# Performance work log

Measured on AMD Instinct MI355X. Metric: run time of the kernel, lower is better.

## Reference

```python
import jax, jax.numpy as jnp
import numpy as np

B, T_SRC, T_TGT, H = 256, 128, 32, 512


def setup_inputs() -> dict:
    key = jax.random.key(0)
    ks = jax.random.split(key, 16)
    bound = 1.0 / np.sqrt(H)  # PyTorch LSTM default init range

    def w(k, *sh):
        return jax.random.uniform(k, sh, jnp.float32, -bound, bound)

    return {
        "src": jax.random.normal(ks[0], (B, T_SRC, 1), jnp.float32),
        # encoder layer 0 (input_dim=1) and layer 1 (input_dim=H); gate order i,f,g,o
        "enc_w_ih0": w(ks[1], 4 * H, 1), "enc_w_hh0": w(ks[2], 4 * H, H), "enc_b0": w(ks[3], 4 * H),
        "enc_w_ih1": w(ks[4], 4 * H, H), "enc_w_hh1": w(ks[5], 4 * H, H), "enc_b1": w(ks[6], 4 * H),
        # decoder layers
        "dec_w_ih0": w(ks[7], 4 * H, 1), "dec_w_hh0": w(ks[8], 4 * H, H), "dec_b0": w(ks[9], 4 * H),
        "dec_w_ih1": w(ks[10], 4 * H, H), "dec_w_hh1": w(ks[11], 4 * H, H), "dec_b1": w(ks[12], 4 * H),
        # output projection Linear(H, 1)
        "proj_w": w(ks[13], 1, H), "proj_b": w(ks[14], 1),
        "tgt_len": T_TGT,
    }


def _cell(gx, h, c, w_hh):
    # gx: precomputed x @ w_ih.T + b; PyTorch gate order i, f, g, o
    gates = gx + h @ w_hh.T
    i, f, g, o = jnp.split(gates, 4, axis=-1)
    c = jax.nn.sigmoid(f) * c + jax.nn.sigmoid(i) * jnp.tanh(g)
    h = jax.nn.sigmoid(o) * jnp.tanh(c)
    return h, c


def _run_layer(xs, w_ih, w_hh, b):
    # xs: (B, T, in) -> (outputs (B,T,H), final h (B,H), final c (B,H))
    Bb, Hh = xs.shape[0], w_hh.shape[1]
    gx = jnp.einsum('bti,gi->btg', xs, w_ih) + b  # hoist input GEMM out of the scan

    def step(carry, g_t):
        h, c = carry
        h, c = _cell(g_t, h, c, w_hh)
        return (h, c), h

    z = jnp.zeros((Bb, Hh), xs.dtype)
    (h, c), hs = jax.lax.scan(step, (z, z), gx.transpose(1, 0, 2))
    return hs.transpose(1, 0, 2), h, c


def reference(src, enc_w_ih0, enc_w_hh0, enc_b0, enc_w_ih1, enc_w_hh1, enc_b1,
              dec_w_ih0, dec_w_hh0, dec_b0, dec_w_ih1, dec_w_hh1, dec_b1,
              proj_w, proj_b, tgt_len):
    # ---- encoder: 2-layer LSTM over src, keep final (h, c) per layer ----
    hs0, h0, c0 = _run_layer(src, enc_w_ih0, enc_w_hh0, enc_b0)
    _, h1, c1 = _run_layer(hs0, enc_w_ih1, enc_w_hh1, enc_b1)

    last = src[:, -1, :]  # (B, 1), last observed value

    def dec_step(carry, _):
        last, h0, c0, h1, c1 = carry
        gx0 = last @ dec_w_ih0.T + dec_b0
        h0, c0 = _cell(gx0, h0, c0, dec_w_hh0)
        gx1 = h0 @ dec_w_ih1.T + dec_b1
        h1, c1 = _cell(gx1, h1, c1, dec_w_hh1)
        y = h1 @ proj_w.T + proj_b  # (B, 1)
        # original feeds out.detach() as the next input
        return (jax.lax.stop_gradient(y), h0, c0, h1, c1), y

    _, ys = jax.lax.scan(dec_step, (last, h0, c0, h1, c1), None, length=tgt_len)
    return ys.transpose(1, 0, 2)  # (B, tgt_len, 1)
```

## Files before the change

### kernel.cpp

```cpp
#include <hip/hip_runtime.h>
#include <cstdint>
#include <cstddef>

#define BN 256
#define HN 512
#define TSN 128
#define TTN 32
#define NSL 16
#define SRN 128

typedef __fp16 f16;
typedef __fp16 f16x8 __attribute__((ext_vector_type(8)));
typedef float  f32x4 __attribute__((ext_vector_type(4)));
typedef float  f32x2 __attribute__((ext_vector_type(2)));
typedef unsigned int u32;
typedef unsigned int u32x2 __attribute__((ext_vector_type(2)));

static constexpr size_t WQ_OFF  = 0;
static constexpr size_t WQ_MAT  = (size_t)NSL*SRN*HN*2;
static constexpr size_t HS0_OFF = WQ_OFF + 6*WQ_MAT;
static constexpr size_t HS_SLOT = (size_t)BN*HN*2;
static constexpr size_t H1_OFF  = HS0_OFF + 129*HS_SLOT;
static constexpr size_t H0_OFF  = H1_OFF + 2*HS_SLOT;
static constexpr size_t YP_OFF  = H0_OFF + 2*HS_SLOT;
static constexpr size_t BAR_OFF = YP_OFF + (size_t)BN*NSL*4;

__device__ __forceinline__ float sigm(float x){ return 1.f/(1.f+__expf(-x)); }
__device__ __forceinline__ float tanh_(float x){
  float t = __expf(-2.f*fabsf(x));
  float r = (1.f-t)/(1.f+t);
  return x<0.f ? -r : r;
}

__device__ __forceinline__ f16x8 ldg16_cv(const f16* p){
  f32x4 r;
  asm volatile("global_load_dwordx4 %0, %1, off sc1" : "=v"(r) : "v"(p));
  return __builtin_bit_cast(f16x8, r);
}
__device__ __forceinline__ f32x2 ldg8f_cv(const float* p){
  f32x2 r;
  asm volatile("global_load_dwordx2 %0, %1, off sc1" : "=v"(r) : "v"(p));
  return r;
}
__device__ __forceinline__ void stg8_cv(f16* p, u32x2 v){
  asm volatile("global_store_dwordx2 %0, %1, off sc1" :: "v"(p), "v"(v) : "memory");
}
__device__ __forceinline__ void stg4f_cv(float* p, float v){
  asm volatile("global_store_dword %0, %1, off sc1" :: "v"(p), "v"(v) : "memory");
}
__device__ __forceinline__ void vmwait(){
  asm volatile("s_waitcnt vmcnt(0)" ::: "memory");
  __builtin_amdgcn_sched_barrier(0);
}
__device__ __forceinline__ void wait_k(const int* fb, int wv, int target){
  const int l = threadIdx.x & 63;
  const int* p = fb + (((wv<<2) | ((l>>2)&3))<<2) + (l&3);
  int v;
  do {
    asm volatile("global_load_dword %0, %1, off sc1\n\ts_waitcnt vmcnt(0)"
                 : "=v"(v) : "v"(p) : "memory");
  } while (!__all(v >= target));
  __builtin_amdgcn_sched_barrier(0);
}
__device__ __forceinline__ void wait_row(const int* fb, int wv, int target){
  const int l = threadIdx.x & 63;
  const int* p = fb + ((l&15)<<2) + wv;
  int v;
  do {
    asm volatile("global_load_dword %0, %1, off sc1\n\ts_waitcnt vmcnt(0)"
                 : "=v"(v) : "v"(p) : "memory");
  } while (!__all(v >= target));
  __builtin_amdgcn_sched_barrier(0);
}
__device__ __forceinline__ void post_wave(int* slot, int v){
  asm volatile("s_waitcnt vmcnt(0)" ::: "memory");
  __builtin_amdgcn_sched_barrier(0);
  if ((threadIdx.x & 63) == 0)
    asm volatile("global_store_dword %0, %1, off sc1" :: "v"(slot), "v"(v) : "memory");
}
__device__ __forceinline__ void post_wave2(int* sa, int va, int* sb, int vb){
  asm volatile("s_waitcnt vmcnt(0)" ::: "memory");
  __builtin_amdgcn_sched_barrier(0);
  if ((threadIdx.x & 63) == 0){
    asm volatile("global_store_dword %0, %1, off sc1" :: "v"(sa), "v"(va) : "memory");
    asm volatile("global_store_dword %0, %1, off sc1" :: "v"(sb), "v"(vb) : "memory");
  }
}

__device__ __forceinline__ void load_bslice(const f16* wsl, int lane, int wv, f16x8 (&bw)[8][4]){
  const int rr = lane & 15;
  const int ko = ((lane>>4)<<3) + wv*128;
  #pragma unroll
  for (int nt=0; nt<8; ++nt){
    const f16* p = wsl + (size_t)(nt*16+rr)*HN + ko;
    #pragma unroll
    for (int kk=0; kk<4; ++kk) bw[nt][kk] = *(const f16x8*)(p + kk*32);
  }
}
template<int MT>
__device__ __forceinline__ void load_a_cv(const f16* ab, int lane, int wv, f16x8 (&A)[MT][4]){
  const int rr = lane & 15;
  const int ko = ((lane>>4)<<3) + wv*128;
  #pragma unroll
  for (int mt=0; mt<MT; ++mt){
    const f16* p = ab + (size_t)(mt*16+rr)*HN + ko;
    #pragma unroll
    for (int kk=0; kk<4; ++kk) A[mt][kk] = ldg16_cv(p + kk*32);
  }
}
__device__ __forceinline__ void mfma_row(const f16x8 (&A)[4], const f16x8 (&bw)[8][4],
                                         f32x4 (&acc)[8]){
  #pragma unroll
  for (int kk=0; kk<4; ++kk)
    #pragma unroll
    for (int nt=0; nt<8; ++nt)
      acc[nt] = __builtin_amdgcn_mfma_f32_16x16x32_f16(A[kk], bw[nt][kk], acc[nt], 0, 0, 0);
}
__device__ __forceinline__ void wpart1(float (*gS)[32][132], const f32x4 (&acc)[8], int lane, int wv, int mt){
  const int c0 = lane & 15, r0 = (lane>>4)*4;
  #pragma unroll
  for (int nt=0; nt<8; ++nt)
    #pragma unroll
    for (int i=0; i<4; ++i)
      gS[wv][mt*16+r0+i][nt*16+c0] = acc[nt][i];
}
__device__ __forceinline__ float gsum(const float (*gS)[32][132], int row, int r){
  return gS[0][row][r] + gS[1][row][r] + gS[2][row][r] + gS[3][row][r];
}

__global__ void k_init(uint8_t* ws){
  const int i = blockIdx.x*256 + threadIdx.x;
  float* a = (float*)(ws + HS0_OFF);
  float* b = (float*)(ws + H1_OFF);
  int*   c = (int*)(ws + BAR_OFF);
  a[i] = 0.f;
  b[i] = 0.f;
  if (i < 2048) c[i] = 0;
}
__global__ void k_wconv(const float* s0, const float* s1, const float* s2,
                        const float* s3, const float* s4, const float* s5, f16* dst){
  const int i = blockIdx.x*256 + threadIdx.x;
  const int k = i & 511, r = (i>>9)&127, j = (i>>16)&15, m = i>>20;
  const float* s = (m==0)?s0:(m==1)?s1:(m==2)?s2:(m==3)?s3:(m==4)?s4:s5;
  const int R = (r>>5)*512 + j*32 + (r&31);
  dst[i] = (f16)s[(size_t)R*HN + k];
}

__global__ void __launch_bounds__(256,1) k_main(
    const float* __restrict__ src,   const float* __restrict__ wih0e, const float* __restrict__ b0e,
    const float* __restrict__ b1e,   const float* __restrict__ wih0d, const float* __restrict__ b0d,
    const float* __restrict__ b1d,   const float* __restrict__ projw, const float* __restrict__ projb,
    uint8_t* __restrict__ ws, float* __restrict__ out)
{
  __shared__ float gS[4][32][132];
  __shared__ float srcS[32][TSN];
  __shared__ float wihS[SRN], bS[SRN], pwS[32], yS[32];

  const int wg = blockIdx.x, tid = threadIdx.x;
  const int lane = tid & 63, wv = tid >> 6;
  const int g = (wg >> 4) & 7, j = wg & 15;
  const bool teamA = (wg < 128);

  const f16* wq = (const f16*)(ws + WQ_OFF);
  f16* hs0 = (f16*)(ws + HS0_OFF);
  f16* h1b = (f16*)(ws + H1_OFF);
  f16* h0b = (f16*)(ws + H0_OFF);
  float* ypb = (float*)(ws + YP_OFF);
  int* F0  = (int*)(ws + BAR_OFF);
  int* F1  = F0 + 512;
  int* FD0 = F0 + 1024;
  int* FD1 = F0 + 1536;
  int* F0g = F0 + g*64, *F1g = F1 + g*64, *FD0g = FD0 + g*64, *FD1g = FD1 + g*64;
  const int fslot = j*4 + wv;

  const int crow = tid >> 3, ckl = (tid & 7)*4;
  float creg[4] = {0.f,0.f,0.f,0.f};

  if (teamA){
    f16x8 bw[8][4];
    load_bslice(wq + (size_t)(0*NSL + j)*SRN*HN, lane, wv, bw);
    for (int i=tid; i<SRN; i+=256){
      int R = (i>>5)*512 + j*32 + (i&31);
      wihS[i] = wih0e[R]; bS[i] = b0e[R];
    }
    for (int i=tid; i<32*TSN; i+=256)
      srcS[i>>7][i&127] = src[(size_t)(g*32 + (i>>7))*TSN + (i&127)];
    __syncthreads();

    for (int t=0; t<TSN; ++t){
      wait_k(F0g, wv, t);
      f16x8 A[2][4];
      load_a_cv<2>(hs0 + (size_t)t*BN*HN + (size_t)g*32*HN, lane, wv, A);
      vmwait();
      f32x4 acc[2][8];
      #pragma unroll
      for (int mt=0; mt<2; ++mt)
        #pragma unroll
        for (int nt=0; nt<8; ++nt) acc[mt][nt] = f32x4{0.f,0.f,0.f,0.f};
      mfma_row(A[0], bw, acc[0]);
      mfma_row(A[1], bw, acc[1]);
      wpart1(gS, acc[0], lane, wv, 0);
      wpart1(gS, acc[1], lane, wv, 1);
      __syncthreads();

      const float xs = srcS[crow][t];
      f16 hv[4];
      #pragma unroll
      for (int q=0; q<4; ++q){
        const int kl = ckl + q;
        float gi = gsum(gS, crow, kl)    + xs*wihS[kl]    + bS[kl];
        float gf = gsum(gS, crow, 32+kl) + xs*wihS[32+kl] + bS[32+kl];
        float gg = gsum(gS, crow, 64+kl) + xs*wihS[64+kl] + bS[64+kl];
        float go = gsum(gS, crow, 96+kl) + xs*wihS[96+kl] + bS[96+kl];
        float cc = sigm(gf)*creg[q] + sigm(gi)*tanh_(gg);
        creg[q] = cc;
        hv[q] = (f16)(sigm(go)*tanh_(cc));
      }
      __syncthreads();

      union { f16 h4[4]; u32x2 u; } pk;
      #pragma unroll
      for (int q=0; q<4; ++q) pk.h4[q] = hv[q];
      stg8_cv(hs0 + (size_t)(t+1)*BN*HN + (size_t)(g*32+crow)*HN + j*32 + ckl, pk.u);
      post_wave(F0g + fslot, t+1);
    }

    load_bslice(wq + (size_t)(3*NSL + j)*SRN*HN, lane, wv, bw);
    for (int i=tid; i<SRN; i+=256){
      int R = (i>>5)*512 + j*32 + (i&31);
      wihS[i] = wih0d[R]; bS[i] = b0d[R];
    }
    const float pb = projb[0];
    __syncthreads();

    for (int t=0; t<TTN; ++t){
      f16x8 A[2][4];
      const f16* hb;
      if (t == 0){ wait_k(F0g, wv, TSN); hb = hs0 + (size_t)TSN*BN*HN + (size_t)g*32*HN; }
      else       { wait_k(FD0g, wv, t);  hb = h0b + (size_t)(t&1)*HS_SLOT/2 + (size_t)g*32*HN; }
      load_a_cv<2>(hb, lane, wv, A);
      vmwait();
      f32x4 acc[2][8];
      #pragma unroll
      for (int mt=0; mt<2; ++mt)
        #pragma unroll
        for (int nt=0; nt<8; ++nt) acc[mt][nt] = f32x4{0.f,0.f,0.f,0.f};
      mfma_row(A[0], bw, acc[0]);
      mfma_row(A[1], bw, acc[1]);
      wpart1(gS, acc[0], lane, wv, 0);
      wpart1(gS, acc[1], lane, wv, 1);
      __syncthreads();

      if (t == 0){
        if (tid < 32) yS[tid] = src[(size_t)(g*32+tid)*TSN + (TSN-1)];
      } else {
        wait_row(FD1g, wv, t);
        f32x2 v2 = ldg8f_cv(ypb + (size_t)(g*32+crow)*NSL + (tid&7)*2);
        vmwait();
        float pp = v2[0] + v2[1];
        pp += __shfl_xor(pp, 1);
        pp += __shfl_xor(pp, 2);
        pp += __shfl_xor(pp, 4);
        if ((tid & 7) == 0){
          float y = pb + pp;
          yS[crow] = y;
          if (j == 0) out[(size_t)(g*32+crow)*TTN + (t-1)] = y;
        }
      }
      __syncthreads();

      const float yv = yS[crow];
      f16 hv[4];
      #pragma unroll
      for (int q=0; q<4; ++q){
        const int kl = ckl + q;
        float gi = gsum(gS, crow, kl)    + yv*wihS[kl]    + bS[kl];
        float gf = gsum(gS, crow, 32+kl) + yv*wihS[32+kl] + bS[32+kl];
        float gg = gsum(gS, crow, 64+kl) + yv*wihS[64+kl] + bS[64+kl];
        float go = gsum(gS, crow, 96+kl) + yv*wihS[96+kl] + bS[96+kl];
        float cc = sigm(gf)*creg[q] + sigm(gi)*tanh_(gg);
        creg[q] = cc;
        hv[q] = (f16)(sigm(go)*tanh_(cc));
      }
      __syncthreads();

      union { f16 h4[4]; u32x2 u; } pk;
      #pragma unroll
      for (int q=0; q<4; ++q) pk.h4[q] = hv[q];
      stg8_cv(h0b + (size_t)((t+1)&1)*HS_SLOT/2 + (size_t)(g*32+crow)*HN + j*32 + ckl, pk.u);
      post_wave(FD0g + fslot, t+1);
    }

    if (j == 0){
      wait_row(FD1g, wv, TTN);
      f32x2 v2 = ldg8f_cv(ypb + (size_t)(g*32+crow)*NSL + (tid&7)*2);
      vmwait();
      float pp = v2[0] + v2[1];
      pp += __shfl_xor(pp, 1);
      pp += __shfl_xor(pp, 2);
      pp += __shfl_xor(pp, 4);
      if ((tid & 7) == 0) out[(size_t)(g*32+crow)*TTN + (TTN-1)] = pb + pp;
    }
  } else {
    f16x8 bwi[8][4], bwh[8][4];
    load_bslice(wq + (size_t)(1*NSL + j)*SRN*HN, lane, wv, bwi);
    load_bslice(wq + (size_t)(2*NSL + j)*SRN*HN, lane, wv, bwh);
    for (int i=tid; i<SRN; i+=256){
      int R = (i>>5)*512 + j*32 + (i&31);
      bS[i] = b1e[R];
    }
    __syncthreads();

    for (int t=0; t<TSN; ++t){
      wait_k(F1g, wv, t);
      f16x8 A[2][4];
      load_a_cv<2>(h1b + (size_t)(t&1)*HS_SLOT/2 + (size_t)g*32*HN, lane, wv, A);
      vmwait();
      f32x4 acc[2][8];
      #pragma unroll
      for (int mt=0; mt<2; ++mt)
        #pragma unroll
        for (int nt=0; nt<8; ++nt) acc[mt][nt] = f32x4{0.f,0.f,0.f,0.f};
      mfma_row(A[0], bwh, acc[0]);
      mfma_row(A[1], bwh, acc[1]);
      wait_k(F0g, wv, t+1);
      f16x8 A2[2][4];
      load_a_cv<2>(hs0 + (size_t)(t+1)*BN*HN + (size_t)g*32*HN, lane, wv, A2);
      vmwait();
      mfma_row(A2[0], bwi, acc[0]);
      mfma_row(A2[1], bwi, acc[1]);
      wpart1(gS, acc[0], lane, wv, 0);
      wpart1(gS, acc[1], lane, wv, 1);
      __syncthreads();

      f16 hv[4];
      #pragma unroll
      for (int q=0; q<4; ++q){
        const int kl = ckl + q;
        float gi = gsum(gS, crow, kl)    + bS[kl];
        float gf = gsum(gS, crow, 32+kl) + bS[32+kl];
        float gg = gsum(gS, crow, 64+kl) + bS[64+kl];
        float go = gsum(gS, crow, 96+kl) + bS[96+kl];
        float cc = sigm(gf)*creg[q] + sigm(gi)*tanh_(gg);
        creg[q] = cc;
        hv[q] = (f16)(sigm(go)*tanh_(cc));
      }
      __syncthreads();

      union { f16 h4[4]; u32x2 u; } pk;
      #pragma unroll
      for (int q=0; q<4; ++q) pk.h4[q] = hv[q];
      stg8_cv(h1b + (size_t)((t+1)&1)*HS_SLOT/2 + (size_t)(g*32+crow)*HN + j*32 + ckl, pk.u);
      post_wave(F1g + fslot, t+1);
    }

    load_bslice(wq + (size_t)(4*NSL + j)*SRN*HN, lane, wv, bwi);
    load_bslice(wq + (size_t)(5*NSL + j)*SRN*HN, lane, wv, bwh);
    for (int i=tid; i<SRN; i+=256){
      int R = (i>>5)*512 + j*32 + (i&31);
      bS[i] = b1d[R];
    }
    if (tid < 32) pwS[tid] = projw[j*32 + tid];
    __syncthreads();

    for (int t=0; t<TTN; ++t){
      wait_k(F1g, wv, TSN + t);
      f16x8 A[2][4];
      load_a_cv<2>(h1b + (size_t)(t&1)*HS_SLOT/2 + (size_t)g*32*HN, lane, wv, A);
      vmwait();
      f32x4 acc[2][8];
      #pragma unroll
      for (int mt=0; mt<2; ++mt)
        #pragma unroll
        for (int nt=0; nt<8; ++nt) acc[mt][nt] = f32x4{0.f,0.f,0.f,0.f};
      mfma_row(A[0], bwh, acc[0]);
      mfma_row(A[1], bwh, acc[1]);
      wait_k(FD0g, wv, t+1);
      f16x8 A2[2][4];
      load_a_cv<2>(h0b + (size_t)((t+1)&1)*HS_SLOT/2 + (size_t)g*32*HN, lane, wv, A2);
      vmwait();
      mfma_row(A2[0], bwi, acc[0]);
      mfma_row(A2[1], bwi, acc[1]);
      wpart1(gS, acc[0], lane, wv, 0);
      wpart1(gS, acc[1], lane, wv, 1);
      __syncthreads();

      f16 hv[4];
      float hvf[4];
      #pragma unroll
      for (int q=0; q<4; ++q){
        const int kl = ckl + q;
        float gi = gsum(gS, crow, kl)    + bS[kl];
        float gf = gsum(gS, crow, 32+kl) + bS[32+kl];
        float gg = gsum(gS, crow, 64+kl) + bS[64+kl];
        float go = gsum(gS, crow, 96+kl) + bS[96+kl];
        float cc = sigm(gf)*creg[q] + sigm(gi)*tanh_(gg);
        creg[q] = cc;
        hvf[q] = sigm(go)*tanh_(cc);
        hv[q] = (f16)hvf[q];
      }
      __syncthreads();

      union { f16 h4[4]; u32x2 u; } pk;
      #pragma unroll
      for (int q=0; q<4; ++q) pk.h4[q] = hv[q];
      stg8_cv(h1b + (size_t)((t+1)&1)*HS_SLOT/2 + (size_t)(g*32+crow)*HN + j*32 + ckl, pk.u);

      float pp = hvf[0]*pwS[ckl] + hvf[1]*pwS[ckl+1] + hvf[2]*pwS[ckl+2] + hvf[3]*pwS[ckl+3];
      pp += __shfl_xor(pp, 1);
      pp += __shfl_xor(pp, 2);
      pp += __shfl_xor(pp, 4);
      if ((tid & 7) == 0) stg4f_cv(ypb + (size_t)(g*32+crow)*NSL + j, pp);
      post_wave2(F1g + fslot, TSN + t + 1, FD1g + fslot, t + 1);
    }
  }
}

extern "C" void kernel_launch(void* const* d_in, const int* in_sizes, int n_in,
                              void* d_out, int out_size, void* d_ws, size_t ws_size,
                              hipStream_t stream)
{
  (void)in_sizes; (void)n_in; (void)out_size; (void)ws_size;
  const float* src   = (const float*)d_in[0];
  const float* wih0e = (const float*)d_in[1];
  const float* hh0e  = (const float*)d_in[2];
  const float* b0e   = (const float*)d_in[3];
  const float* ih1e  = (const float*)d_in[4];
  const float* hh1e  = (const float*)d_in[5];
  const float* b1e   = (const float*)d_in[6];
  const float* wih0d = (const float*)d_in[7];
  const float* hh0d  = (const float*)d_in[8];
  const float* b0d   = (const float*)d_in[9];
  const float* ih1d  = (const float*)d_in[10];
  const float* hh1d  = (const float*)d_in[11];
  const float* b1d   = (const float*)d_in[12];
  const float* projw = (const float*)d_in[13];
  const float* projb = (const float*)d_in[14];
  uint8_t* ws = (uint8_t*)d_ws;
  float* out = (float*)d_out;

  k_init<<<dim3(256), dim3(256), 0, stream>>>(ws);
  k_wconv<<<dim3(6*NSL*SRN*HN/256), dim3(256), 0, stream>>>(hh0e, ih1e, hh1e, hh0d, ih1d, hh1d,
                                                            (f16*)(ws + WQ_OFF));
  k_main<<<dim3(256), dim3(256), 0, stream>>>(src, wih0e, b0e, b1e, wih0d, b0d, b1d,
                                              projw, projb, ws, out);
}
```

Before: 1.300 ms.

## Remap workgroups so batch groups share an XCD and use L2-scope coherence

Swaps the workgroup-to-(g,j) mapping so the 32 blocks of one batch group land on the same XCD under round-robin dispatch. At startup each block publishes its XCC id and checks whether all members of its group share it. If they do, all flag polling, hidden-state loads and stores use sc0 (L2-coherent) instead of sc1 (system/LLC scope), which is meant to cut cross-step synchronisation latency. The check needs an extra global handshake and flag slots, and relies on blocks being co-resident and dispatched in the expected pattern.

Result: slower. 1.692 ms (+30.1%).

```diff
diff --git a/kernel.cpp b/kernel.cpp
--- a/kernel.cpp
+++ b/kernel.cpp
@@ -32,59 +32,74 @@
   return x<0.f ? -r : r;
 }
 
-__device__ __forceinline__ f16x8 ldg16_cv(const f16* p){
+__device__ __forceinline__ f16x8 ld_h16(const f16* p, bool llc){
   f32x4 r;
-  asm volatile("global_load_dwordx4 %0, %1, off sc1" : "=v"(r) : "v"(p));
+  if (llc) asm volatile("global_load_dwordx4 %0, %1, off sc1" : "=v"(r) : "v"(p));
+  else     asm volatile("global_load_dwordx4 %0, %1, off sc0" : "=v"(r) : "v"(p));
   return __builtin_bit_cast(f16x8, r);
 }
-__device__ __forceinline__ f32x2 ldg8f_cv(const float* p){
+__device__ __forceinline__ f32x2 ld_f8(const float* p, bool llc){
   f32x2 r;
-  asm volatile("global_load_dwordx2 %0, %1, off sc1" : "=v"(r) : "v"(p));
+  if (llc) asm volatile("global_load_dwordx2 %0, %1, off sc1" : "=v"(r) : "v"(p));
+  else     asm volatile("global_load_dwordx2 %0, %1, off sc0" : "=v"(r) : "v"(p));
   return r;
 }
-__device__ __forceinline__ void stg8_cv(f16* p, u32x2 v){
-  asm volatile("global_store_dwordx2 %0, %1, off sc1" :: "v"(p), "v"(v) : "memory");
-}
-__device__ __forceinline__ void stg4f_cv(float* p, float v){
-  asm volatile("global_store_dword %0, %1, off sc1" :: "v"(p), "v"(v) : "memory");
+__device__ __forceinline__ void st_h8(f16* p, u32x2 v, bool llc){
+  if (llc) asm volatile("global_store_dwordx2 %0, %1, off sc1" :: "v"(p), "v"(v) : "memory");
+  else     asm volatile("global_store_dwordx2 %0, %1, off sc0" :: "v"(p), "v"(v) : "memory");
+}
+__device__ __forceinline__ void st_f4(float* p, float v, bool llc){
+  if (llc) asm volatile("global_store_dword %0, %1, off sc1" :: "v"(p), "v"(v) : "memory");
+  else     asm volatile("global_store_dword %0, %1, off sc0" :: "v"(p), "v"(v) : "memory");
+}
+__device__ __forceinline__ void st_i4(int* p, int v, bool llc){
+  if (llc) asm volatile("global_store_dword %0, %1, off sc1" :: "v"(p), "v"(v) : "memory");
+  else     asm volatile("global_store_dword %0, %1, off sc0" :: "v"(p), "v"(v) : "memory");
+}
+__device__ __forceinline__ int ld_i4_llc(const int* p){
+  int v;
+  asm volatile("global_load_dword %0, %1, off sc1\n\ts_waitcnt vmcnt(0)"
+               : "=v"(v) : "v"(p) : "memory");
+  __builtin_amdgcn_sched_barrier(0);
+  return v;
 }
 __device__ __forceinline__ void vmwait(){
   asm volatile("s_waitcnt vmcnt(0)" ::: "memory");
   __builtin_amdgcn_sched_barrier(0);
 }
-__device__ __forceinline__ void wait_k(const int* fb, int wv, int target){
+__device__ __forceinline__ void wait_k(const int* fb, int wv, int target, bool llc){
   const int l = threadIdx.x & 63;
   const int* p = fb + (((wv<<2) | ((l>>2)&3))<<2) + (l&3);
   int v;
-  do {
-    asm volatile("global_load_dword %0, %1, off sc1\n\ts_waitcnt vmcnt(0)"
-                 : "=v"(v) : "v"(p) : "memory");
-  } while (!__all(v >= target));
+  if (llc){
+    do { asm volatile("global_load_dword %0, %1, off sc1\n\ts_waitcnt vmcnt(0)"
+                      : "=v"(v) : "v"(p) : "memory"); } while (!__all(v >= target));
+  } else {
+    do { asm volatile("global_load_dword %0, %1, off sc0\n\ts_waitcnt vmcnt(0)"
+                      : "=v"(v) : "v"(p) : "memory"); } while (!__all(v >= target));
+  }
   __builtin_amdgcn_sched_barrier(0);
 }
-__device__ __forceinline__ void wait_row(const int* fb, int wv, int target){
+__device__ __forceinline__ void wait_row(const int* fb, int wv, int target, bool llc){
   const int l = threadIdx.x & 63;
   const int* p = fb + ((l&15)<<2) + wv;
   int v;
-  do {
-    asm volatile("global_load_dword %0, %1, off sc1\n\ts_waitcnt vmcnt(0)"
-                 : "=v"(v) : "v"(p) : "memory");
-  } while (!__all(v >= target));
+  if (llc){
+    do { asm volatile("global_load_dword %0, %1, off sc1\n\ts_waitcnt vmcnt(0)"
+                      : "=v"(v) : "v"(p) : "memory"); } while (!__all(v >= target));
+  } else {
+    do { asm volatile("global_load_dword %0, %1, off sc0\n\ts_waitcnt vmcnt(0)"
+                      : "=v"(v) : "v"(p) : "memory"); } while (!__all(v >= target));
+  }
   __builtin_amdgcn_sched_barrier(0);
 }
-__device__ __forceinline__ void post_wave(int* slot, int v){
-  asm volatile("s_waitcnt vmcnt(0)" ::: "memory");
-  __builtin_amdgcn_sched_barrier(0);
-  if ((threadIdx.x & 63) == 0)
-    asm volatile("global_store_dword %0, %1, off sc1" :: "v"(slot), "v"(v) : "memory");
-}
-__device__ __forceinline__ void post_wave2(int* sa, int va, int* sb, int vb){
-  asm volatile("s_waitcnt vmcnt(0)" ::: "memory");
-  __builtin_amdgcn_sched_barrier(0);
-  if ((threadIdx.x & 63) == 0){
-    asm volatile("global_store_dword %0, %1, off sc1" :: "v"(sa), "v"(va) : "memory");
-    asm volatile("global_store_dword %0, %1, off sc1" :: "v"(sb), "v"(vb) : "memory");
-  }
+__device__ __forceinline__ void post_wave(int* slot, int v, bool llc){
+  vmwait();
+  if ((threadIdx.x & 63) == 0) st_i4(slot, v, llc);
+}
+__device__ __forceinline__ void post_wave2(int* sa, int va, int* sb, int vb, bool llc){
+  vmwait();
+  if ((threadIdx.x & 63) == 0){ st_i4(sa, va, llc); st_i4(sb, vb, llc); }
 }
 
 __device__ __forceinline__ void load_bslice(const f16* wsl, int lane, int wv, f16x8 (&bw)[8][4]){
@@ -98,14 +113,14 @@
   }
 }
 template<int MT>
-__device__ __forceinline__ void load_a_cv(const f16* ab, int lane, int wv, f16x8 (&A)[MT][4]){
+__device__ __forceinline__ void load_a_cv(const f16* ab, int lane, int wv, f16x8 (&A)[MT][4], bool llc){
   const int rr = lane & 15;
   const int ko = ((lane>>4)<<3) + wv*128;
   #pragma unroll
   for (int mt=0; mt<MT; ++mt){
     const f16* p = ab + (size_t)(mt*16+rr)*HN + ko;
     #pragma unroll
-    for (int kk=0; kk<4; ++kk) A[mt][kk] = ldg16_cv(p + kk*32);
+    for (int kk=0; kk<4; ++kk) A[mt][kk] = ld_h16(p + kk*32, llc);
   }
 }
 __device__ __forceinline__ void mfma_row(const f16x8 (&A)[4], const f16x8 (&bw)[8][4],
@@ -135,7 +150,7 @@
   int*   c = (int*)(ws + BAR_OFF);
   a[i] = 0.f;
   b[i] = 0.f;
-  if (i < 2048) c[i] = 0;
+  if (i < 2304) c[i] = 0;
 }
 __global__ void k_wconv(const float* s0, const float* s1, const float* s2,
                         const float* s3, const float* s4, const float* s5, f16* dst){
@@ -155,10 +170,11 @@
   __shared__ float gS[4][32][132];
   __shared__ float srcS[32][TSN];
   __shared__ float wihS[SRN], bS[SRN], pwS[32], yS[32];
+  __shared__ int llcS;
 
   const int wg = blockIdx.x, tid = threadIdx.x;
   const int lane = tid & 63, wv = tid >> 6;
-  const int g = (wg >> 4) & 7, j = wg & 15;
+  const int g = wg & 7, j = (wg >> 3) & 15;
   const bool teamA = (wg < 128);
 
   const f16* wq = (const f16*)(ws + WQ_OFF);
@@ -170,8 +186,28 @@
   int* F1  = F0 + 512;
   int* FD0 = F0 + 1024;
   int* FD1 = F0 + 1536;
+  int* xslots = F0 + 2048;
   int* F0g = F0 + g*64, *F1g = F1 + g*64, *FD0g = FD0 + g*64, *FD1g = FD1 + g*64;
   const int fslot = j*4 + wv;
+
+  {
+    const int xcc = __builtin_amdgcn_s_getreg(63508) & 0xf;
+    if (tid == 0){
+      asm volatile("global_store_dword %0, %1, off sc1" :: "v"(xslots + wg), "v"(xcc + 1) : "memory");
+      asm volatile("s_waitcnt vmcnt(0)" ::: "memory");
+    }
+    if (tid < 32){
+      const int member = (tid < 16) ? (tid*8 + g) : (128 + (tid-16)*8 + g);
+      const int* p = xslots + member;
+      int v;
+      do { v = ld_i4_llc(p); } while (v == 0);
+      const bool same = (v == xcc + 1) || (tid >= 32);
+      unsigned long long m = __ballot(same);
+      if (tid == 0) llcS = (m == ~0ull) ? 0 : 1;
+    }
+    __syncthreads();
+  }
+  const bool llc = (__builtin_amdgcn_readfirstlane(llcS) != 0);
 
   const int crow = tid >> 3, ckl = (tid & 7)*4;
   float creg[4] = {0.f,0.f,0.f,0.f};
@@ -188,9 +224,9 @@
     __syncthreads();
 
     for (int t=0; t<TSN; ++t){
-      wait_k(F0g, wv, t);
+      wait_k(F0g, wv, t, llc);
       f16x8 A[2][4];
-      load_a_cv<2>(hs0 + (size_t)t*BN*HN + (size_t)g*32*HN, lane, wv, A);
+      load_a_cv<2>(hs0 + (size_t)t*BN*HN + (size_t)g*32*HN, lane, wv, A, llc);
       vmwait();
       f32x4 acc[2][8];
       #pragma unroll
@@ -221,8 +257,8 @@
       union { f16 h4[4]; u32x2 u; } pk;
       #pragma unroll
       for (int q=0; q<4; ++q) pk.h4[q] = hv[q];
-      stg8_cv(hs0 + (size_t)(t+1)*BN*HN + (size_t)(g*32+crow)*HN + j*32 + ckl, pk.u);
-      post_wave(F0g + fslot, t+1);
+      st_h8(hs0 + (size_t)(t+1)*BN*HN + (size_t)(g*32+crow)*HN + j*32 + ckl, pk.u, llc);
+      post_wave(F0g + fslot, t+1, llc);
     }
 
     load_bslice(wq + (size_t)(3*NSL + j)*SRN*HN, lane, wv, bw);
@@ -236,9 +272,9 @@
     for (int t=0; t<TTN; ++t){
       f16x8 A[2][4];
       const f16* hb;
-      if (t == 0){ wait_k(F0g, wv, TSN); hb = hs0 + (size_t)TSN*BN*HN + (size_t)g*32*HN; }
-      else       { wait_k(FD0g, wv, t);  hb = h0b + (size_t)(t&1)*HS_SLOT/2 + (size_t)g*32*HN; }
-      load_a_cv<2>(hb, lane, wv, A);
+      if (t == 0){ wait_k(F0g, wv, TSN, llc); hb = hs0 + (size_t)TSN*BN*HN + (size_t)g*32*HN; }
+      else       { wait_k(FD0g, wv, t, llc);  hb = h0b + (size_t)(t&1)*HS_SLOT/2 + (size_t)g*32*HN; }
+      load_a_cv<2>(hb, lane, wv, A, llc);
       vmwait();
       f32x4 acc[2][8];
       #pragma unroll
@@ -254,8 +290,8 @@
       if (t == 0){
         if (tid < 32) yS[tid] = src[(size_t)(g*32+tid)*TSN + (TSN-1)];
       } else {
-        wait_row(FD1g, wv, t);
-        f32x2 v2 = ldg8f_cv(ypb + (size_t)(g*32+crow)*NSL + (tid&7)*2);
+        wait_row(FD1g, wv, t, llc);
+        f32x2 v2 = ld_f8(ypb + (size_t)(g*32+crow)*NSL + (tid&7)*2, llc);
         vmwait();
         float pp = v2[0] + v2[1];
         pp += __shfl_xor(pp, 1);
@@ -287,13 +323,13 @@
       union { f16 h4[4]; u32x2 u; } pk;
       #pragma unroll
       for (int q=0; q<4; ++q) pk.h4[q] = hv[q];
-      stg8_cv(h0b + (size_t)((t+1)&1)*HS_SLOT/2 + (size_t)(g*32+crow)*HN + j*32 + ckl, pk.u);
-      post_wave(FD0g + fslot, t+1);
+      st_h8(h0b + (size_t)((t+1)&1)*HS_SLOT/2 + (size_t)(g*32+crow)*HN + j*32 + ckl, pk.u, llc);
+      post_wave(FD0g + fslot, t+1, llc);
     }
 
     if (j == 0){
-      wait_row(FD1g, wv, TTN);
-      f32x2 v2 = ldg8f_cv(ypb + (size_t)(g*32+crow)*NSL + (tid&7)*2);
+      wait_row(FD1g, wv, TTN, llc);
+      f32x2 v2 = ld_f8(ypb + (size_t)(g*32+crow)*NSL + (tid&7)*2, llc);
       vmwait();
       float pp = v2[0] + v2[1];
       pp += __shfl_xor(pp, 1);
@@ -312,9 +348,9 @@
     __syncthreads();
 
     for (int t=0; t<TSN; ++t){
-      wait_k(F1g, wv, t);
+      wait_k(F1g, wv, t, llc);
       f16x8 A[2][4];
-      load_a_cv<2>(h1b + (size_t)(t&1)*HS_SLOT/2 + (size_t)g*32*HN, lane, wv, A);
+      load_a_cv<2>(h1b + (size_t)(t&1)*HS_SLOT/2 + (size_t)g*32*HN, lane, wv, A, llc);
       vmwait();
       f32x4 acc[2][8];
       #pragma unroll
@@ -323,9 +359,9 @@
         for (int nt=0; nt<8; ++nt) acc[mt][nt] = f32x4{0.f,0.f,0.f,0.f};
       mfma_row(A[0], bwh, acc[0]);
       mfma_row(A[1], bwh, acc[1]);
-      wait_k(F0g, wv, t+1);
+      wait_k(F0g, wv, t+1, llc);
       f16x8 A2[2][4];
-      load_a_cv<2>(hs0 + (size_t)(t+1)*BN*HN + (size_t)g*32*HN, lane, wv, A2);
+      load_a_cv<2>(hs0 + (size_t)(t+1)*BN*HN + (size_t)g*32*HN, lane, wv, A2, llc);
       vmwait();
       mfma_row(A2[0], bwi, acc[0]);
       mfma_row(A2[1], bwi, acc[1]);
@@ -350,8 +386,8 @@
       union { f16 h4[4]; u32x2 u; } pk;
       #pragma unroll
       for (int q=0; q<4; ++q) pk.h4[q] = hv[q];
-      stg8_cv(h1b + (size_t)((t+1)&1)*HS_SLOT/2 + (size_t)(g*32+crow)*HN + j*32 + ckl, pk.u);
-      post_wave(F1g + fslot, t+1);
+      st_h8(h1b + (size_t)((t+1)&1)*HS_SLOT/2 + (size_t)(g*32+crow)*HN + j*32 + ckl, pk.u, llc);
+      post_wave(F1g + fslot, t+1, llc);
     }
 
     load_bslice(wq + (size_t)(4*NSL + j)*SRN*HN, lane, wv, bwi);
@@ -364,9 +400,9 @@
     __syncthreads();
 
     for (int t=0; t<TTN; ++t){
-      wait_k(F1g, wv, TSN + t);
+      wait_k(F1g, wv, TSN + t, llc);
       f16x8 A[2][4];
-      load_a_cv<2>(h1b + (size_t)(t&1)*HS_SLOT/2 + (size_t)g*32*HN, lane, wv, A);
+      load_a_cv<2>(h1b + (size_t)(t&1)*HS_SLOT/2 + (size_t)g*32*HN, lane, wv, A, llc);
       vmwait();
       f32x4 acc[2][8];
       #pragma unroll
@@ -375,9 +411,9 @@
         for (int nt=0; nt<8; ++nt) acc[mt][nt] = f32x4{0.f,0.f,0.f,0.f};
       mfma_row(A[0], bwh, acc[0]);
       mfma_row(A[1], bwh, acc[1]);
-      wait_k(FD0g, wv, t+1);
+      wait_k(FD0g, wv, t+1, llc);
       f16x8 A2[2][4];
-      load_a_cv<2>(h0b + (size_t)((t+1)&1)*HS_SLOT/2 + (size_t)g*32*HN, lane, wv, A2);
+      load_a_cv<2>(h0b + (size_t)((t+1)&1)*HS_SLOT/2 + (size_t)g*32*HN, lane, wv, A2, llc);
       vmwait();
       mfma_row(A2[0], bwi, acc[0]);
       mfma_row(A2[1], bwi, acc[1]);
@@ -404,14 +440,14 @@
       union { f16 h4[4]; u32x2 u; } pk;
       #pragma unroll
       for (int q=0; q<4; ++q) pk.h4[q] = hv[q];
-      stg8_cv(h1b + (size_t)((t+1)&1)*HS_SLOT/2 + (size_t)(g*32+crow)*HN + j*32 + ckl, pk.u);
+      st_h8(h1b + (size_t)((t+1)&1)*HS_SLOT/2 + (size_t)(g*32+crow)*HN + j*32 + ckl, pk.u, llc);
 
       float pp = hvf[0]*pwS[ckl] + hvf[1]*pwS[ckl+1] + hvf[2]*pwS[ckl+2] + hvf[3]*pwS[ckl+3];
       pp += __shfl_xor(pp, 1);
       pp += __shfl_xor(pp, 2);
       pp += __shfl_xor(pp, 4);
-      if ((tid & 7) == 0) stg4f_cv(ypb + (size_t)(g*32+crow)*NSL + j, pp);
-      post_wave2(F1g + fslot, TSN + t + 1, FD1g + fslot, t + 1);
+      if ((tid & 7) == 0) st_f4(ypb + (size_t)(g*32+crow)*NSL + j, pp, llc);
+      post_wave2(F1g + fslot, TSN + t + 1, FD1g + fslot, t + 1, llc);
     }
   }
 }
```
